# Performance work log

Hardware: AMD Instinct MI355X
Metric: run time of the kernel (lower is better)

Reference implementation:

```python
import jax, jax.numpy as jnp
import numpy as np

GROUP_SIZE = 128


def dequant_rtn(qweight, scale, zero_point):
    # qweight: [O, I] int, scale/zero_point: [O, I//GROUP_SIZE]
    O, I = qweight.shape
    G = scale.shape[1]
    gs = I // G
    q = qweight.reshape(O, G, gs).astype(jnp.float32)
    zp = zero_point.astype(jnp.float32)[:, :, None]
    w = (q - zp) * scale[:, :, None]
    return w.reshape(O, I)


def setup_inputs() -> dict:
    key = jax.random.key(0)
    k1, k2, k3, k4, k5 = jax.random.split(key, 5)
    B, S, I, O = 2, 2048, 4096, 11008
    G = I // GROUP_SIZE
    x = jax.random.normal(k1, (B, S, I), dtype=jnp.float32)
    qweight = jax.random.randint(k2, (O, I), 0, 16, dtype=jnp.int32)
    scale = jax.random.uniform(k3, (O, G), dtype=jnp.float32) * 0.02 + 1e-3
    zero_point = jax.random.randint(k4, (O, G), 0, 16, dtype=jnp.int32)
    bias = jax.random.normal(k5, (O,), dtype=jnp.float32)
    return {"x": x, "qweight": qweight, "scale": scale,
            "zero_point": zero_point, "bias": bias}


def reference(x, qweight, scale, zero_point, bias):
    # weight-only path: dequant weight, then F.linear(x, w, bias)
    w = dequant_rtn(qweight, scale, zero_point)  # [O, I] fp32
    return jnp.einsum('bsi,oi->bso', x, w) + bias
```

## Files before the change

kernel.cpp:

```cpp
#include <hip/hip_runtime.h>
#include <cstdint>
#include <cstddef>

typedef __attribute__((ext_vector_type(4))) int i32x4;
typedef __bf16 bf16;
typedef __attribute__((ext_vector_type(8))) __bf16 bf16x8;
typedef __attribute__((ext_vector_type(4))) float f32x4;

#define BM 128
#define BN 128
#define BKB 128
#define GROUP_M 16
#define GM256 4
#define NXCD 8

__device__ __forceinline__ unsigned bf16_rne(float f) {
  unsigned u = __float_as_uint(f);
  unsigned r = 0x7FFFu + ((u >> 16) & 1u);
  return ((u + r) >> 16) & 0xFFFFu;
}
__device__ __forceinline__ unsigned pack2(float a, float b) {
  return bf16_rne(a) | (bf16_rne(b) << 16);
}
__device__ __forceinline__ int pack4i8(int a, int b, int c, int d) {
  return (a & 0xFF) | ((b & 0xFF) << 8) | ((c & 0xFF) << 16) | (d << 24);
}
__device__ __forceinline__ int q_i8(float v) {
  v = fminf(fmaxf(v, -127.0f), 127.0f);
  return __float2int_rn(v);
}

__global__ __launch_bounds__(256) void prep_kernel(
    const float* __restrict__ x, char* __restrict__ xq, float* __restrict__ xscale,
    int M,
    const int* __restrict__ q, const float* __restrict__ scale,
    const int* __restrict__ zp, char* __restrict__ wq, float* __restrict__ wscale,
    int K, int G) {
  __shared__ float red[4];
  const int b = blockIdx.x;
  const int tid = threadIdx.x;
  float f[16];

  if (b < M) {
    const float4* src = (const float4*)(x + (size_t)b * K);
#pragma unroll
    for (int i = 0; i < 4; ++i) {
      float4 v = src[tid + 256 * i];
      f[4 * i + 0] = v.x; f[4 * i + 1] = v.y;
      f[4 * i + 2] = v.z; f[4 * i + 3] = v.w;
    }
  } else {
    const int row = b - M;
    const int4* src = (const int4*)(q + (size_t)row * K);
    const float* srow = scale + (size_t)row * G;
    const int*   zrow = zp + (size_t)row * G;
#pragma unroll
    for (int i = 0; i < 4; ++i) {
      const int j = tid + 256 * i;
      const int g = j >> 5;
      const float s = srow[g];
      const float nzs = -s * (float)zrow[g];
      int4 qv = src[j];
      f[4 * i + 0] = fmaf((float)qv.x, s, nzs);
      f[4 * i + 1] = fmaf((float)qv.y, s, nzs);
      f[4 * i + 2] = fmaf((float)qv.z, s, nzs);
      f[4 * i + 3] = fmaf((float)qv.w, s, nzs);
    }
  }

  float m = 0.f;
#pragma unroll
  for (int j = 0; j < 16; ++j) m = fmaxf(m, fabsf(f[j]));
#pragma unroll
  for (int off = 32; off >= 1; off >>= 1) m = fmaxf(m, __shfl_xor(m, off));
  if ((tid & 63) == 0) red[tid >> 6] = m;
  __syncthreads();
  m = fmaxf(fmaxf(red[0], red[1]), fmaxf(red[2], red[3]));

  const float inv = m > 0.f ? 127.0f / m : 0.f;
  int pk[4];
#pragma unroll
  for (int i = 0; i < 4; ++i)
    pk[i] = pack4i8(q_i8(f[4 * i + 0] * inv), q_i8(f[4 * i + 1] * inv),
                    q_i8(f[4 * i + 2] * inv), q_i8(f[4 * i + 3] * inv));

  char* dst = (b < M) ? (xq + (size_t)b * K) : (wq + (size_t)(b - M) * K);
  int* dst_i32 = (int*)dst;
#pragma unroll
  for (int i = 0; i < 4; ++i) dst_i32[tid + 256 * i] = pk[i];

  if (tid == 0) {
    if (b < M) xscale[b] = m * (1.0f / 127.0f);
    else       wscale[b - M] = m * (1.0f / 127.0f);
  }
}

typedef __attribute__((address_space(1))) void gas_void;
typedef __attribute__((address_space(3))) void las_void;

__device__ __forceinline__ void load_lds16(const void* g, void* l) {
  __builtin_amdgcn_global_load_lds((gas_void*)g, (las_void*)l, 16, 0, 0);
}


#define STAGE_A_H(buf, h, ktb) do {                                           \
    load_lds16(A + abase + (size_t)(ktb) + aoff0 + (size_t)(h) * 64 * K,      \
               &Al[buf][(h) * 8192 + dw]);                                    \
    load_lds16(A + abase + (size_t)(ktb) + aoff1 + (size_t)(h) * 64 * K,      \
               &Al[buf][16384 + (h) * 8192 + dw]);                            \
  } while (0)

#define STAGE_B_H(buf, h, ktb) do {                                           \
    load_lds16(Bw + bbase + (size_t)(ktb) + boff0 + (size_t)(h) * 32 * K,     \
               &Bl[buf][(h) * 16384 + dw]);                                   \
    load_lds16(Bw + bbase + (size_t)(ktb) + boff1 + (size_t)(h) * 32 * K,     \
               &Bl[buf][(h) * 16384 + 8192 + dw]);                            \
  } while (0)

#define PHASE(CUR, MH, NH, STAGE_STMT, WAIT_STMT) do {                        \
    i32x4 afr[4][2], bfr[2][2];                                               \
    _Pragma("unroll")                                                         \
    for (int tm = 0; tm < 4; ++tm) {                                          \
      _Pragma("unroll")                                                       \
      for (int ks = 0; ks < 2; ++ks) {                                        \
        int row = wmb + (MH) * 64 + tm * 16 + l16;                            \
        int kq  = ks * 4 + quad;                                              \
        afr[tm][ks] =                                                         \
            *(const i32x4*)&Al[CUR][(row * 8 + (kq ^ (row & 7))) * 16];       \
      }                                                                       \
    }                                                                         \
    _Pragma("unroll")                                                         \
    for (int tn = 0; tn < 2; ++tn) {                                          \
      _Pragma("unroll")                                                       \
      for (int ks = 0; ks < 2; ++ks) {                                        \
        int p  = (NH) * 128 + wq3 * 32 + tn * 16 + l16;                       \
        int kq = ks * 4 + quad;                                               \
        bfr[tn][ks] =                                                         \
            *(const i32x4*)&Bl[CUR][(p * 8 + (kq ^ (p & 7))) * 16];           \
      }                                                                       \
    }                                                                         \
    STAGE_STMT;                                                               \
    __builtin_amdgcn_s_barrier();                                             \
    asm volatile("s_waitcnt lgkmcnt(0)" ::: "memory");                        \
    __builtin_amdgcn_sched_barrier(0);                                        \
    __builtin_amdgcn_s_setprio(1);                                            \
    _Pragma("unroll")                                                         \
    for (int tm = 0; tm < 4; ++tm) {                                          \
      _Pragma("unroll")                                                       \
      for (int tn = 0; tn < 2; ++tn) {                                        \
        _Pragma("unroll")                                                     \
        for (int ks = 0; ks < 2; ++ks) {                                      \
          acc[(MH) * 4 + tm][(NH) * 2 + tn] =                                 \
              __builtin_amdgcn_mfma_i32_16x16x64_i8(                          \
                  afr[tm][ks], bfr[tn][ks],                                   \
                  acc[(MH) * 4 + tm][(NH) * 2 + tn], 0, 0, 0);                \
        }                                                                     \
      }                                                                       \
    }                                                                         \
    __builtin_amdgcn_s_setprio(0);                                            \
    WAIT_STMT;                                                                \
    __builtin_amdgcn_s_barrier();                                             \
    __builtin_amdgcn_sched_barrier(0);                                        \
  } while (0)

__global__ __launch_bounds__(512) void gemm_i8_256(
    const char* __restrict__ A,
    const char* __restrict__ Bw,
    const float* __restrict__ ascale,
    const float* __restrict__ bscale,
    const float* __restrict__ bias,
    float* __restrict__ C,
    int M, int N, int K) {
  __shared__ __align__(16) char Al[2][256 * 128];
  __shared__ __align__(16) char Bl[2][256 * 128];
  const int tid  = threadIdx.x;
  const int wave = tid >> 6;
  const int lane = tid & 63;
  const int quad = lane >> 4;
  const int l16  = lane & 15;
  const int wq3  = wave & 3;
  const int wmb  = (wave >> 2) * 128;
  const int wnb  = wq3 * 64;

  const int nbm = M / 256, nbn = N / 256;
  const int cpx = (nbm * nbn) / NXCD;
  const int swz = ((int)blockIdx.x % NXCD) * cpx + (int)blockIdx.x / NXCD;
  const int per_group = GM256 * nbn;
  const int gid = swz / per_group;
  const int rem = swz - gid * per_group;
  int gm = nbm - gid * GM256; if (gm > GM256) gm = GM256;
  const int bm = (gid * GM256 + (rem % gm)) * 256;
  const int bn = (rem / gm) * 256;

  const int r0 = tid >> 3;
  const int kq16 = (((tid & 7) ^ (r0 & 7)) * 16);
  const size_t aoff0 = (size_t)r0 * K + kq16;
  const size_t aoff1 = aoff0 + (size_t)128 * K;
  const size_t boff0 = (size_t)((r0 >> 5) * 64 + (r0 & 31)) * K + kq16;
  const size_t boff1 = boff0 + (size_t)128 * K;
  const int dw = wave * 1024;
  const size_t abase = (size_t)bm * K;
  const size_t bbase = (size_t)bn * K;
  const int NT = K / 128;

  i32x4 acc[8][4];
#pragma unroll
  for (int i = 0; i < 8; ++i)
#pragma unroll
    for (int j = 0; j < 4; ++j)
      acc[i][j] = (i32x4){0, 0, 0, 0};

  STAGE_A_H(0, 0, 0);
  STAGE_A_H(0, 1, 0);
  STAGE_B_H(0, 0, 0);
  STAGE_B_H(0, 1, 0);
  STAGE_B_H(1, 0, 128);
  STAGE_A_H(1, 0, 128);
  asm volatile("s_waitcnt vmcnt(4)" ::: "memory");
  __builtin_amdgcn_s_barrier();
  __builtin_amdgcn_sched_barrier(0);

  for (int t = 0; t < NT; ++t) {
    const int cur = t & 1;
    const int nxt = cur ^ 1;
    const int kt1 = (t + 1) * 128;
    const int kt2 = (t + 2) * 128;
    const bool s1 = (t + 1) < NT;
    const bool s2 = (t + 2) < NT;

    PHASE(cur, 0, 0, { if (s1) STAGE_A_H(nxt, 1, kt1); }, {});
    PHASE(cur, 1, 0, { if (s1) STAGE_B_H(nxt, 1, kt1); }, {});
    PHASE(cur, 0, 1, { if (s2) STAGE_B_H(cur, 0, kt2); }, {});
    PHASE(cur, 1, 1, { if (s2) STAGE_A_H(cur, 0, kt2); },
          {
            if (s2) { asm volatile("s_waitcnt vmcnt(4)" ::: "memory"); }
            else    { asm volatile("s_waitcnt vmcnt(0)" ::: "memory"); }
          });
  }

#pragma unroll
  for (int tn = 0; tn < 4; ++tn) {
    int col = bn + wnb + tn * 16 + l16;
    float bv = bias[col];
    float ws = bscale[col];
#pragma unroll
    for (int tm = 0; tm < 8; ++tm) {
      int row0 = bm + wmb + tm * 16 + quad * 4;
#pragma unroll
      for (int v = 0; v < 4; ++v) {
        float val = ascale[row0 + v] * ws * (float)acc[tm][tn][v] + bv;
        __builtin_nontemporal_store(val, &C[(size_t)(row0 + v) * N + col]);
      }
    }
  }
}

__global__ __launch_bounds__(256) void gemm_i8_kernel(
    const char* __restrict__ A, const char* __restrict__ Bw,
    const float* __restrict__ ascale, const float* __restrict__ bscale,
    const float* __restrict__ bias, float* __restrict__ C,
    int M, int N, int K) {
  __shared__ __align__(16) char Alds[BM * BKB];
  __shared__ __align__(16) char Blds[BN * BKB];
  const int tid  = threadIdx.x;
  const int wave = tid >> 6;
  const int lane = tid & 63;
  const int quad = lane >> 4;
  const int l16  = lane & 15;

  const int nbm = M / BM;
  const int nbn = N / BN;
  int flat = blockIdx.x;
  int per_group = GROUP_M * nbn;
  int gid = flat / per_group;
  int rem = flat - gid * per_group;
  int gm = nbm - gid * GROUP_M;
  if (gm > GROUP_M) gm = GROUP_M;
  const int bm = (gid * GROUP_M + (rem % gm)) * BM;
  const int bn = (rem / gm) * BN;

  const int wm = (wave & 1) * 64;
  const int wn = (wave >> 1) * 64;

  i32x4 acc[4][4];
#pragma unroll
  for (int i = 0; i < 4; ++i)
#pragma unroll
    for (int j = 0; j < 4; ++j)
      acc[i][j] = (i32x4){0, 0, 0, 0};

  for (int kt = 0; kt < K; kt += BKB) {
#pragma unroll
    for (int t = 0; t < 4; ++t) {
      int s0 = (wave * 4 + t) * 64;
      int s  = s0 + lane;
      int m  = s >> 3;
      int kq = (s & 7) ^ (m & 7);
      load_lds16(A  + (size_t)(bm + m) * K + kt + kq * 16, &Alds[s0 * 16]);
      load_lds16(Bw + (size_t)(bn + m) * K + kt + kq * 16, &Blds[s0 * 16]);
    }
    __syncthreads();

#pragma unroll
    for (int ks = 0; ks < 2; ++ks) {
      i32x4 af[4], bfr[4];
#pragma unroll
      for (int tm = 0; tm < 4; ++tm) {
        int m  = wm + tm * 16 + l16;
        int kq = ks * 4 + quad;
        af[tm] = *(const i32x4*)&Alds[(m * 8 + (kq ^ (m & 7))) * 16];
      }
#pragma unroll
      for (int tn = 0; tn < 4; ++tn) {
        int n  = wn + tn * 16 + l16;
        int kq = ks * 4 + quad;
        bfr[tn] = *(const i32x4*)&Blds[(n * 8 + (kq ^ (n & 7))) * 16];
      }
#pragma unroll
      for (int tm = 0; tm < 4; ++tm)
#pragma unroll
        for (int tn = 0; tn < 4; ++tn)
          acc[tm][tn] = __builtin_amdgcn_mfma_i32_16x16x64_i8(
              af[tm], bfr[tn], acc[tm][tn], 0, 0, 0);
    }
    __syncthreads();
  }

#pragma unroll
  for (int tn = 0; tn < 4; ++tn) {
    int col = bn + wn + tn * 16 + l16;
    float bv = bias[col];
    float ws = bscale[col];
#pragma unroll
    for (int tm = 0; tm < 4; ++tm) {
      int row0 = bm + wm + tm * 16 + quad * 4;
#pragma unroll
      for (int v = 0; v < 4; ++v) {
        float val = ascale[row0 + v] * ws * (float)acc[tm][tn][v] + bv;
        __builtin_nontemporal_store(val, &C[(size_t)(row0 + v) * N + col]);
      }
    }
  }
}

__global__ __launch_bounds__(256) void gemm_fused_kernel(
    const float* __restrict__ X, const int* __restrict__ Q,
    const float* __restrict__ scale, const int* __restrict__ zp,
    const float* __restrict__ bias, float* __restrict__ C,
    int M, int N, int K, int G) {
  __shared__ __align__(16) bf16 Alds[128 * 64];
  __shared__ __align__(16) bf16 Blds[128 * 64];
  const int tid  = threadIdx.x;
  const int wave = tid >> 6;
  const int lane = tid & 63;
  const int quad = lane >> 4;
  const int l16  = lane & 15;
  const int bm = blockIdx.y * 128;
  const int bn = blockIdx.x * 128;
  const int wm = (wave & 1) * 64;
  const int wn = (wave >> 1) * 64;

  f32x4 acc[4][4];
#pragma unroll
  for (int i = 0; i < 4; ++i)
#pragma unroll
    for (int j = 0; j < 4; ++j)
      acc[i][j] = (f32x4){0.f, 0.f, 0.f, 0.f};

  for (int kt = 0; kt < K; kt += 64) {
#pragma unroll
    for (int i = 0; i < 4; ++i) {
      int c = tid + i * 256;
      int m = c >> 3;
      int kq = (c & 7) ^ (m & 7);
      const float* src = X + (size_t)(bm + m) * K + kt + kq * 8;
      float4 v0 = *(const float4*)src;
      float4 v1 = *(const float4*)(src + 4);
      uint4 p;
      p.x = pack2(v0.x, v0.y); p.y = pack2(v0.z, v0.w);
      p.z = pack2(v1.x, v1.y); p.w = pack2(v1.z, v1.w);
      *(uint4*)&Alds[c * 8] = p;
    }
#pragma unroll
    for (int i = 0; i < 4; ++i) {
      int c = tid + i * 256;
      int n = c >> 3;
      int kq = (c & 7) ^ (n & 7);
      int kcol = kt + kq * 8;
      size_t row = (size_t)(bn + n);
      int g = kcol >> 7;
      float s = scale[row * G + g];
      float z = (float)zp[row * G + g];
      const int* src = Q + row * K + kcol;
      int4 q0 = *(const int4*)src;
      int4 q1 = *(const int4*)(src + 4);
      uint4 p;
      p.x = pack2(((float)q0.x - z) * s, ((float)q0.y - z) * s);
      p.y = pack2(((float)q0.z - z) * s, ((float)q0.w - z) * s);
      p.z = pack2(((float)q1.x - z) * s, ((float)q1.y - z) * s);
      p.w = pack2(((float)q1.z - z) * s, ((float)q1.w - z) * s);
      *(uint4*)&Blds[c * 8] = p;
    }
    __syncthreads();

#pragma unroll
    for (int ks = 0; ks < 2; ++ks) {
      bf16x8 af[4], bfr[4];
#pragma unroll
      for (int tm = 0; tm < 4; ++tm) {
        int m  = wm + tm * 16 + l16;
        int kq = ks * 4 + quad;
        af[tm] = *(const bf16x8*)&Alds[(m * 8 + (kq ^ (m & 7))) * 8];
      }
#pragma unroll
      for (int tn = 0; tn < 4; ++tn) {
        int n  = wn + tn * 16 + l16;
        int kq = ks * 4 + quad;
        bfr[tn] = *(const bf16x8*)&Blds[(n * 8 + (kq ^ (n & 7))) * 8];
      }
#pragma unroll
      for (int tm = 0; tm < 4; ++tm)
#pragma unroll
        for (int tn = 0; tn < 4; ++tn)
          acc[tm][tn] = __builtin_amdgcn_mfma_f32_16x16x32_bf16(
              af[tm], bfr[tn], acc[tm][tn], 0, 0, 0);
    }
    __syncthreads();
  }

#pragma unroll
  for (int tn = 0; tn < 4; ++tn) {
    int col = bn + wn + tn * 16 + l16;
    float bv = bias[col];
#pragma unroll
    for (int tm = 0; tm < 4; ++tm) {
      int row0 = bm + wm + tm * 16 + quad * 4;
#pragma unroll
      for (int v = 0; v < 4; ++v)
        C[(size_t)(row0 + v) * N + col] = acc[tm][tn][v] + bv;
    }
  }
}

extern "C" void kernel_launch(void* const* d_in, const int* in_sizes, int n_in,
                              void* d_out, int out_size, void* d_ws, size_t ws_size,
                              hipStream_t stream) {
  const float* x     = (const float*)d_in[0];
  const int*   qw    = (const int*)d_in[1];
  const float* scale = (const float*)d_in[2];
  const int*   zp    = (const int*)d_in[3];
  const float* bias  = (const float*)d_in[4];
  float* out = (float*)d_out;

  const int O = in_sizes[4];
  const int I = (int)(in_sizes[1] / O);
  const int M = (int)(in_sizes[0] / I);
  const int G = in_sizes[2] / O;
  const int K = I, N = O;

  size_t off_xq = 0;
  size_t off_xs = off_xq + (size_t)M * K;
  size_t off_wq = (off_xs + (size_t)M * 4 + 255) & ~(size_t)255;
  size_t off_ws_ = off_wq + (size_t)N * K;
  size_t need   = ((off_ws_ + (size_t)N * 4 + 255) & ~(size_t)255);

  if (ws_size >= need && K == 4096) {
    char*  xq = (char*)d_ws + off_xq;
    float* xs = (float*)((char*)d_ws + off_xs);
    char*  wq = (char*)d_ws + off_wq;
    float* wsc = (float*)((char*)d_ws + off_ws_);

    prep_kernel<<<M + N, 256, 0, stream>>>(x, xq, xs, M, qw, scale, zp, wq, wsc, K, G);

    const int nb256 = (M / 256) * (N / 256);
    if ((M % 256) == 0 && (N % 256) == 0 && (nb256 % NXCD) == 0) {
      gemm_i8_256<<<nb256, 512, 0, stream>>>(xq, wq, xs, wsc, bias, out, M, N, K);
    } else {
      int nblocks = (M / BM) * (N / BN);
      gemm_i8_kernel<<<nblocks, 256, 0, stream>>>(xq, wq, xs, wsc, bias, out, M, N, K);
    }
  } else {
    dim3 gemm_grid((unsigned)(N / 128), (unsigned)(M / 128));
    gemm_fused_kernel<<<gemm_grid, 256, 0, stream>>>(x, qw, scale, zp, bias, out,
                                                     M, N, K, G);
  }
}
```

Before: 563.2 us.

## Restructure int8 GEMM main loop into two k-slice phases with simple double buffering

Replaces the four M/N-quadrant phases with two phases that each cover the whole 256x256 tile for one k-slice. All four next-tile loads are issued in the first phase, and the loop waits for them with vmcnt(0) at the end of the iteration. This drops the deeper prefetch, where part of tile t+2 was loaded into the current buffer. The new order reuses each loaded A/B fragment across more MFMAs and uses fewer barriers, but it shrinks the prefetch distance and holds more fragment registers live.

```diff
diff --git a/kernel.cpp b/kernel.cpp
--- a/kernel.cpp
+++ b/kernel.cpp
@@ -117,27 +117,19 @@
                &Bl[buf][(h) * 16384 + 8192 + dw]);                            \
   } while (0)
 
-#define PHASE(CUR, MH, NH, STAGE_STMT, WAIT_STMT) do {                        \
-    i32x4 afr[4][2], bfr[2][2];                                               \
+#define PHASE2(CUR, KS, STAGE_STMT, WAIT_STMT) do {                           \
+    i32x4 afr[8], bfr[4];                                                     \
     _Pragma("unroll")                                                         \
-    for (int tm = 0; tm < 4; ++tm) {                                          \
-      _Pragma("unroll")                                                       \
-      for (int ks = 0; ks < 2; ++ks) {                                        \
-        int row = wmb + (MH) * 64 + tm * 16 + l16;                            \
-        int kq  = ks * 4 + quad;                                              \
-        afr[tm][ks] =                                                         \
-            *(const i32x4*)&Al[CUR][(row * 8 + (kq ^ (row & 7))) * 16];       \
-      }                                                                       \
+    for (int tm = 0; tm < 8; ++tm) {                                          \
+      int row = wmb + tm * 16 + l16;                                          \
+      int kq  = (KS) * 4 + quad;                                              \
+      afr[tm] = *(const i32x4*)&Al[CUR][(row * 8 + (kq ^ (row & 7))) * 16];   \
     }                                                                         \
     _Pragma("unroll")                                                         \
-    for (int tn = 0; tn < 2; ++tn) {                                          \
-      _Pragma("unroll")                                                       \
-      for (int ks = 0; ks < 2; ++ks) {                                        \
-        int p  = (NH) * 128 + wq3 * 32 + tn * 16 + l16;                       \
-        int kq = ks * 4 + quad;                                               \
-        bfr[tn][ks] =                                                         \
-            *(const i32x4*)&Bl[CUR][(p * 8 + (kq ^ (p & 7))) * 16];           \
-      }                                                                       \
+    for (int j = 0; j < 4; ++j) {                                             \
+      int p  = (j >> 1) * 128 + wq3 * 32 + (j & 1) * 16 + l16;                \
+      int kq = (KS) * 4 + quad;                                               \
+      bfr[j] = *(const i32x4*)&Bl[CUR][(p * 8 + (kq ^ (p & 7))) * 16];        \
     }                                                                         \
     STAGE_STMT;                                                               \
     __builtin_amdgcn_s_barrier();                                             \
@@ -145,16 +137,11 @@
     __builtin_amdgcn_sched_barrier(0);                                        \
     __builtin_amdgcn_s_setprio(1);                                            \
     _Pragma("unroll")                                                         \
-    for (int tm = 0; tm < 4; ++tm) {                                          \
+    for (int tm = 0; tm < 8; ++tm) {                                          \
       _Pragma("unroll")                                                       \
-      for (int tn = 0; tn < 2; ++tn) {                                        \
-        _Pragma("unroll")                                                     \
-        for (int ks = 0; ks < 2; ++ks) {                                      \
-          acc[(MH) * 4 + tm][(NH) * 2 + tn] =                                 \
-              __builtin_amdgcn_mfma_i32_16x16x64_i8(                          \
-                  afr[tm][ks], bfr[tn][ks],                                   \
-                  acc[(MH) * 4 + tm][(NH) * 2 + tn], 0, 0, 0);                \
-        }                                                                     \
+      for (int j = 0; j < 4; ++j) {                                           \
+        acc[tm][j] = __builtin_amdgcn_mfma_i32_16x16x64_i8(                   \
+            afr[tm], bfr[j], acc[tm][j], 0, 0, 0);                            \
       }                                                                       \
     }                                                                         \
     __builtin_amdgcn_s_setprio(0);                                            \
@@ -214,9 +201,7 @@
   STAGE_A_H(0, 1, 0);
   STAGE_B_H(0, 0, 0);
   STAGE_B_H(0, 1, 0);
-  STAGE_B_H(1, 0, 128);
-  STAGE_A_H(1, 0, 128);
-  asm volatile("s_waitcnt vmcnt(4)" ::: "memory");
+  asm volatile("s_waitcnt vmcnt(0)" ::: "memory");
   __builtin_amdgcn_s_barrier();
   __builtin_amdgcn_sched_barrier(0);
 
@@ -224,18 +209,20 @@
     const int cur = t & 1;
     const int nxt = cur ^ 1;
     const int kt1 = (t + 1) * 128;
-    const int kt2 = (t + 2) * 128;
     const bool s1 = (t + 1) < NT;
-    const bool s2 = (t + 2) < NT;
-
-    PHASE(cur, 0, 0, { if (s1) STAGE_A_H(nxt, 1, kt1); }, {});
-    PHASE(cur, 1, 0, { if (s1) STAGE_B_H(nxt, 1, kt1); }, {});
-    PHASE(cur, 0, 1, { if (s2) STAGE_B_H(cur, 0, kt2); }, {});
-    PHASE(cur, 1, 1, { if (s2) STAGE_A_H(cur, 0, kt2); },
-          {
-            if (s2) { asm volatile("s_waitcnt vmcnt(4)" ::: "memory"); }
-            else    { asm volatile("s_waitcnt vmcnt(0)" ::: "memory"); }
-          });
+
+    PHASE2(cur, 0,
+           {
+             if (s1) {
+               STAGE_A_H(nxt, 0, kt1);
+               STAGE_A_H(nxt, 1, kt1);
+               STAGE_B_H(nxt, 0, kt1);
+               STAGE_B_H(nxt, 1, kt1);
+             }
+           },
+           {});
+    PHASE2(cur, 1, {},
+           { asm volatile("s_waitcnt vmcnt(0)" ::: "memory"); });
   }
 
 #pragma unroll
```

Result: faster. 546.3 us (-3.0%).
